# Performance work log

Measured on AMD Instinct MI355X. Metric: run time of the kernel, lower is better.

Reference implementation:

```python
import jax, jax.numpy as jnp
import numpy as np

# ---- module hyperparameters (init_kwargs) ----
QMIN, QMAX, QBINS = -8.0, 8.0, 128
PMIN, PMAX, PBINS = -10.0, 10.0, 128
GAMMA_F = 1.0
N_TRAJ = 16384


def _grid():
    # x = arange(qmin - 4/gamma_f, qmax + 4/gamma_f + 0.1/maxp, 0.1/maxp)
    maxp = max(abs(PMIN), abs(PMAX))
    step = 0.1 / maxp
    x = np.arange(QMIN - 4.0 / GAMMA_F, QMAX + 4.0 / GAMMA_F + step, step)
    return x.astype(np.float32)


def setup_inputs() -> dict:
    key = jax.random.key(0)
    ks = jax.random.split(key, 6)
    shape = (1, N_TRAJ)
    x = jnp.asarray(_grid())
    # psi buffer: stand-in for np.interp(x, spl.x, spl.psis[-1][1]) -- a
    # localized oscillatory wavefunction sampled on the grid.
    psi = (jnp.exp(-0.5 * (x - 1.0) ** 2) * jnp.cos(2.0 * x)).astype(jnp.float32)
    return {
        "factors_re": jax.random.normal(ks[0], shape, jnp.float32),
        "factors_im": jax.random.normal(ks[1], shape, jnp.float32),
        "q_re": jax.random.normal(ks[2], shape, jnp.float32),
        "q_im": 0.5 * jax.random.normal(ks[3], shape, jnp.float32),
        "p_re": jax.random.normal(ks[4], shape, jnp.float32),
        "p_im": 0.5 * jax.random.normal(ks[5], shape, jnp.float32),
        "x": x,
        "psi": psi,
    }


def _trapz0(y, x):
    # trapezoid rule along axis 0; y: [M, N] (complex), x: [M]
    dx = jnp.diff(x)
    return jnp.sum(0.5 * (y[1:] + y[:-1]) * dx[:, None], axis=0)


def _forward(factors_re, factors_im, q_re, q_im, p_re, p_im, x, psi):
    g = GAMMA_F
    factors = factors_re + 1j * factors_im  # [1, N] complex
    # _calc_proj: xi = 2*g*q + 1j*p ; qf = Re(xi)/(2g), pf = Im(xi)
    qf = q_re - p_im / (2.0 * g)
    pf = 2.0 * g * q_im + p_re
    dq = (QMAX - QMIN) / QBINS
    dp = (PMAX - PMIN) / PBINS
    qb = jnp.floor((qf - QMIN) / dq)
    pb = jnp.floor((pf - PMIN) / dp)
    bins = (qb * PBINS + pb).astype(jnp.int32).reshape(-1)  # [N]
    n = bins.shape[0]
    # torch: enumerate(torch.unique(bins)) -> rank among sorted unique values.
    # jnp.unique inverse (size=n, large fill pads at the end) gives the same map.
    _, inv = jnp.unique(bins, return_inverse=True, size=n, fill_value=jnp.int32(2**30))
    inds = inv.reshape(qf.shape)  # [1, N] compact bin ids
    qc = (qb + 0.5) * dq + QMIN  # bin centers [1, N]
    pc = (pb + 0.5) * dp + PMIN
    # _gf: coherent-state Gaussians on grid x -> [M, N]
    norm = (2.0 * g / jnp.pi) ** 0.25
    dxq = x[:, None] - qc.reshape(-1)[None, :]  # [M, N]
    gfs = norm * jnp.exp(-g * dxq * dxq + 1j * pc.reshape(-1)[None, :] * dxq)
    gt = _trapz0(jnp.conj(gfs) * psi[:, None], x)  # [N] complex
    # _calc_pref (reconstruction): exponential prefactor that can blow up,
    # hence the nan_to_num + clamp in the original.
    pref = norm * jnp.exp(g * q_im * q_im + 1j * (p_re * q_im))  # [1, N]
    pref = (jnp.clip(jnp.nan_to_num(pref.real), -100.0, 100.0)
            + 1j * jnp.clip(jnp.nan_to_num(pref.imag), -100.0, 100.0))
    vals = pref * factors  # [1, N]
    b = vals.shape[0]
    binned = jnp.zeros_like(vals).at[jnp.arange(b)[:, None], inds].add(vals)
    loss = jnp.sum(jnp.abs(binned - gt[None, :]) ** 2)
    return jnp.sqrt(loss)


def reference(factors_re, factors_im, q_re, q_im, p_re, p_im, x, psi):
    return _forward(factors_re, factors_im, q_re, q_im, p_re, p_im, x, psi)
```

## Files before the change

### kernel.cpp

```cpp
#include <hip/hip_runtime.h>
#include <math.h>


#define PRES_BITS  65536
#define PRES_WORDS 1024
#define PRES_OFF   32768
#define CHUNKS     16

__global__ void prep_kernel(const float* __restrict__ f_re, const float* __restrict__ f_im,
                            const float* __restrict__ q_re, const float* __restrict__ q_im,
                            const float* __restrict__ p_re, const float* __restrict__ p_im,
                            float* __restrict__ qc, float* __restrict__ pc,
                            float* __restrict__ vre, float* __restrict__ vim,
                            int* __restrict__ bins, unsigned long long* __restrict__ pres, int n)
{
    int i = blockIdx.x * blockDim.x + threadIdx.x;
    if (i >= n) return;
    const float norm = 0.8932438417380023f;
    float qi = q_im[i], pr = p_re[i];
    float qf = q_re[i] - 0.5f * p_im[i];
    float pf = 2.0f * qi + pr;
    float qb = floorf((qf - (-8.0f)) / 0.125f);
    float pb = floorf((pf - (-10.0f)) / 0.15625f);
    int b = (int)(qb * 128.0f + pb);
    bins[i] = b;
    int pidx = min(max(b + PRES_OFF, 0), PRES_BITS - 1);
    atomicOr(&pres[pidx >> 6], 1ull << (pidx & 63));
    qc[i] = (qb + 0.5f) * 0.125f + (-8.0f);
    pc[i] = (pb + 0.5f) * 0.15625f + (-10.0f);
    float ea = norm * expf(qi * qi);
    float s, c;
    __sincosf(pr * qi, &s, &c);
    float prr = fminf(fmaxf(ea * c, -100.0f), 100.0f);
    float pri = fminf(fmaxf(ea * s, -100.0f), 100.0f);
    float fr = f_re[i], fi = f_im[i];
    vre[i] = prr * fr - pri * fi;
    vim[i] = prr * fi + pri * fr;
}

__global__ void wpsi_kernel(const float* __restrict__ x, const float* __restrict__ psi,
                            float* __restrict__ wpsi, int M)
{
    int m = blockIdx.x * blockDim.x + threadIdx.x;
    if (m >= M) return;
    float w;
    if (m == 0)            w = 0.5f * (x[1] - x[0]);
    else if (m == M - 1)   w = 0.5f * (x[M - 1] - x[M - 2]);
    else                   w = 0.5f * (x[m + 1] - x[m - 1]);
    wpsi[m] = w * psi[m] * 0.8932438417380023f;
}

__global__ void scan_kernel(const unsigned long long* __restrict__ pres, int* __restrict__ base)
{
    __shared__ int partials[PRES_WORDS];
    int t = threadIdx.x;
    int c = __popcll(pres[t]);
    partials[t] = c;
    __syncthreads();
    for (int off = 1; off < PRES_WORDS; off <<= 1) {
        int v = (t >= off) ? partials[t - off] : 0;
        __syncthreads();
        partials[t] += v;
        __syncthreads();
    }
    base[t] = partials[t] - c;
}

__global__ void scatter_kernel(const int* __restrict__ bins,
                               const unsigned long long* __restrict__ pres,
                               const int* __restrict__ base,
                               const float* __restrict__ vre, const float* __restrict__ vim,
                               float* __restrict__ bre, float* __restrict__ bim, int n)
{
    int i = blockIdx.x * blockDim.x + threadIdx.x;
    if (i >= n) return;
    int pidx = min(max(bins[i] + PRES_OFF, 0), PRES_BITS - 1);
    int w = pidx >> 6, bit = pidx & 63;
    unsigned long long below = pres[w] & ((bit == 0) ? 0ull : (~0ull >> (64 - bit)));
    int cid = base[w] + __popcll(below);
    atomicAdd(&bre[cid], vre[i]);
    atomicAdd(&bim[cid], vim[i]);
}

__global__ void gt_kernel(const float* __restrict__ x, const float* __restrict__ wpsi,
                          const float* __restrict__ qc, const float* __restrict__ pc,
                          float* __restrict__ gre, float* __restrict__ gim,
                          int n, int M, int chunk)
{
    int t = blockIdx.x * blockDim.x + threadIdx.x;
    if (t >= n) return;
    float qcn = qc[t], pcn = pc[t];
    int m0 = blockIdx.y * chunk;
    int m1 = min(m0 + chunk, M);
    float sre = 0.0f, sim = 0.0f;
#pragma unroll 4
    for (int m = m0; m < m1; m++) {
        float xm = x[m], wm = wpsi[m];
        float dxq = xm - qcn;
        float e = __expf(-dxq * dxq) * wm;
        float s, c;
        __sincosf(pcn * dxq, &s, &c);
        sre = fmaf(e, c, sre);
        sim = fmaf(-e, s, sim);
    }
    atomicAdd(&gre[t], sre);
    atomicAdd(&gim[t], sim);
}

__global__ void loss_kernel(const float* __restrict__ gre, const float* __restrict__ gim,
                            const float* __restrict__ bre, const float* __restrict__ bim,
                            float* __restrict__ loss, int n)
{
    int t = blockIdx.x * blockDim.x + threadIdx.x;
    float v = 0.0f;
    if (t < n) {
        float dre = bre[t] - gre[t];
        float dim = bim[t] - gim[t];
        v = dre * dre + dim * dim;
    }
#pragma unroll
    for (int off = 32; off > 0; off >>= 1) v += __shfl_down(v, off);
    __shared__ float l[4];
    int wv = threadIdx.x >> 6, ln = threadIdx.x & 63;
    if (ln == 0) l[wv] = v;
    __syncthreads();
    if (threadIdx.x == 0)
        atomicAdd(loss, l[0] + l[1] + l[2] + l[3]);
}

__global__ void finalize_kernel(const float* __restrict__ loss, float* __restrict__ out)
{
    out[0] = sqrtf(loss[0]);
}

extern "C" void kernel_launch(void* const* d_in, const int* in_sizes, int n_in,
                              void* d_out, int out_size, void* d_ws, size_t ws_size,
                              hipStream_t stream)
{
    const float* f_re = (const float*)d_in[0];
    const float* f_im = (const float*)d_in[1];
    const float* q_re = (const float*)d_in[2];
    const float* q_im = (const float*)d_in[3];
    const float* p_re = (const float*)d_in[4];
    const float* p_im = (const float*)d_in[5];
    const float* x    = (const float*)d_in[6];
    const float* psi  = (const float*)d_in[7];
    int n = in_sizes[0];
    int M = in_sizes[6];

    float* wsf  = (float*)d_ws;
    float* qc   = wsf;
    float* pc   = qc + n;
    float* vre  = pc + n;
    float* vim  = vre + n;
    int*   bins = (int*)(vim + n);
    float* wpsi = (float*)(bins + n);
    int*   base = (int*)(wpsi + 4096);
    float* bre  = (float*)(base + PRES_WORDS);
    float* bim  = bre + n;
    float* gre  = bim + n;
    float* gim  = gre + n;
    unsigned long long* pres = (unsigned long long*)(gim + n);
    float* loss = (float*)(pres + PRES_WORDS);

    hipMemsetAsync(bre, 0, (size_t)(4 * n + 2 * PRES_WORDS + 1) * sizeof(float), stream);

    int chunk = (M + CHUNKS - 1) / CHUNKS;
    prep_kernel<<<(n + 255) / 256, 256, 0, stream>>>(f_re, f_im, q_re, q_im, p_re, p_im,
                                                     qc, pc, vre, vim, bins, pres, n);
    wpsi_kernel<<<(M + 255) / 256, 256, 0, stream>>>(x, psi, wpsi, M);
    scan_kernel<<<1, PRES_WORDS, 0, stream>>>(pres, base);
    scatter_kernel<<<(n + 255) / 256, 256, 0, stream>>>(bins, pres, base, vre, vim, bre, bim, n);
    gt_kernel<<<dim3((n + 255) / 256, CHUNKS), 256, 0, stream>>>(x, wpsi, qc, pc, gre, gim,
                                                                 n, M, chunk);
    loss_kernel<<<(n + 255) / 256, 256, 0, stream>>>(gre, gim, bre, bim, loss, n);
    finalize_kernel<<<1, 1, 0, stream>>>(loss, (float*)d_out);
}
```

Before: 123.4 us.

## Window the Gaussian overlap sum and fold small kernels into fewer launches

```diff
diff --git a/kernel.cpp b/kernel.cpp
--- a/kernel.cpp
+++ b/kernel.cpp
@@ -2,20 +2,32 @@
 #include <math.h>
 
 
+#define PRES_WORDS 1024
 #define PRES_BITS  65536
-#define PRES_WORDS 1024
 #define PRES_OFF   32768
 #define CHUNKS     16
+#define WINR       4.5f
 
 __global__ void prep_kernel(const float* __restrict__ f_re, const float* __restrict__ f_im,
                             const float* __restrict__ q_re, const float* __restrict__ q_im,
                             const float* __restrict__ p_re, const float* __restrict__ p_im,
+                            const float* __restrict__ x, const float* __restrict__ psi,
                             float* __restrict__ qc, float* __restrict__ pc,
                             float* __restrict__ vre, float* __restrict__ vim,
-                            int* __restrict__ bins, unsigned long long* __restrict__ pres, int n)
+                            int* __restrict__ bins, unsigned long long* __restrict__ pres,
+                            float* __restrict__ bre, float* __restrict__ bim,
+                            float2* __restrict__ xw, int n, int M)
 {
     int i = blockIdx.x * blockDim.x + threadIdx.x;
     if (i >= n) return;
+    bre[i] = 0.0f; bim[i] = 0.0f;
+    if (i < M) {
+        float w;
+        if (i == 0)          w = 0.5f * (x[1] - x[0]);
+        else if (i == M - 1) w = 0.5f * (x[M - 1] - x[M - 2]);
+        else                 w = 0.5f * (x[i + 1] - x[i - 1]);
+        xw[i] = make_float2(x[i], w * psi[i] * 0.8932438417380023f);
+    }
     const float norm = 0.8932438417380023f;
     float qi = q_im[i], pr = p_re[i];
     float qf = q_re[i] - 0.5f * p_im[i];
@@ -38,84 +50,85 @@
     vim[i] = prr * fi + pri * fr;
 }
 
-__global__ void wpsi_kernel(const float* __restrict__ x, const float* __restrict__ psi,
-                            float* __restrict__ wpsi, int M)
-{
-    int m = blockIdx.x * blockDim.x + threadIdx.x;
-    if (m >= M) return;
-    float w;
-    if (m == 0)            w = 0.5f * (x[1] - x[0]);
-    else if (m == M - 1)   w = 0.5f * (x[M - 1] - x[M - 2]);
-    else                   w = 0.5f * (x[m + 1] - x[m - 1]);
-    wpsi[m] = w * psi[m] * 0.8932438417380023f;
-}
-
-__global__ void scan_kernel(const unsigned long long* __restrict__ pres, int* __restrict__ base)
-{
-    __shared__ int partials[PRES_WORDS];
-    int t = threadIdx.x;
-    int c = __popcll(pres[t]);
-    partials[t] = c;
-    __syncthreads();
-    for (int off = 1; off < PRES_WORDS; off <<= 1) {
-        int v = (t >= off) ? partials[t - off] : 0;
-        __syncthreads();
-        partials[t] += v;
-        __syncthreads();
-    }
-    base[t] = partials[t] - c;
-}
-
 __global__ void scatter_kernel(const int* __restrict__ bins,
                                const unsigned long long* __restrict__ pres,
-                               const int* __restrict__ base,
                                const float* __restrict__ vre, const float* __restrict__ vim,
                                float* __restrict__ bre, float* __restrict__ bim, int n)
 {
-    int i = blockIdx.x * blockDim.x + threadIdx.x;
+    __shared__ int lbase[PRES_WORDS];
+    int tid = threadIdx.x;
+    if (tid < 64) {
+        int cum[16];
+        int tot = 0;
+        for (int k = 0; k < 16; k++) {
+            cum[k] = tot;
+            tot += __popcll(pres[tid * 16 + k]);
+        }
+        int run = tot;
+        for (int off = 1; off < 64; off <<= 1) {
+            int up = __shfl_up(run, off);
+            if (tid >= off) run += up;
+        }
+        int excl = run - tot;
+        for (int k = 0; k < 16; k++) lbase[tid * 16 + k] = excl + cum[k];
+    }
+    __syncthreads();
+    int i = blockIdx.x * blockDim.x + tid;
     if (i >= n) return;
     int pidx = min(max(bins[i] + PRES_OFF, 0), PRES_BITS - 1);
     int w = pidx >> 6, bit = pidx & 63;
     unsigned long long below = pres[w] & ((bit == 0) ? 0ull : (~0ull >> (64 - bit)));
-    int cid = base[w] + __popcll(below);
+    int cid = lbase[w] + __popcll(below);
     atomicAdd(&bre[cid], vre[i]);
     atomicAdd(&bim[cid], vim[i]);
 }
 
-__global__ void gt_kernel(const float* __restrict__ x, const float* __restrict__ wpsi,
+__global__ void gt_kernel(const float2* __restrict__ xw, const float* __restrict__ x,
                           const float* __restrict__ qc, const float* __restrict__ pc,
-                          float* __restrict__ gre, float* __restrict__ gim,
-                          int n, int M, int chunk)
+                          float* __restrict__ gpre, float* __restrict__ gpim,
+                          int n, int M)
 {
     int t = blockIdx.x * blockDim.x + threadIdx.x;
     if (t >= n) return;
     float qcn = qc[t], pcn = pc[t];
-    int m0 = blockIdx.y * chunk;
-    int m1 = min(m0 + chunk, M);
+    float x0f = x[0];
+    float flo = (qcn - WINR - x0f) * 100.0f;
+    float fhi = (qcn + WINR - x0f) * 100.0f;
+    int mlo = max(0, (int)flo - 1);
+    int mhi = min(M, (int)fhi + 2);
+    int len = mhi - mlo; if (len < 0) len = 0;
+    int c = blockIdx.y;
+    int ms = mlo + (len * c) / CHUNKS;
+    int me = mlo + (len * (c + 1)) / CHUNKS;
     float sre = 0.0f, sim = 0.0f;
-#pragma unroll 4
-    for (int m = m0; m < m1; m++) {
-        float xm = x[m], wm = wpsi[m];
-        float dxq = xm - qcn;
-        float e = __expf(-dxq * dxq) * wm;
-        float s, c;
-        __sincosf(pcn * dxq, &s, &c);
-        sre = fmaf(e, c, sre);
+    for (int m = ms; m < me; m++) {
+        float2 xm = xw[m];
+        float dxq = xm.x - qcn;
+        float e = __expf(-dxq * dxq) * xm.y;
+        float s, cc;
+        __sincosf(pcn * dxq, &s, &cc);
+        sre = fmaf(e, cc, sre);
         sim = fmaf(-e, s, sim);
     }
-    atomicAdd(&gre[t], sre);
-    atomicAdd(&gim[t], sim);
+    gpre[c * n + t] = sre;
+    gpim[c * n + t] = sim;
 }
 
-__global__ void loss_kernel(const float* __restrict__ gre, const float* __restrict__ gim,
-                            const float* __restrict__ bre, const float* __restrict__ bim,
-                            float* __restrict__ loss, int n)
+__global__ void loss_final_kernel(const float* __restrict__ gpre, const float* __restrict__ gpim,
+                                  const float* __restrict__ bre, const float* __restrict__ bim,
+                                  float* __restrict__ loss, int* __restrict__ donecnt,
+                                  float* __restrict__ out, int n)
 {
     int t = blockIdx.x * blockDim.x + threadIdx.x;
     float v = 0.0f;
     if (t < n) {
-        float dre = bre[t] - gre[t];
-        float dim = bim[t] - gim[t];
+        float sre = 0.0f, sim = 0.0f;
+        for (int c = 0; c < CHUNKS; c++) {
+            sre += gpre[c * n + t];
+            sim += gpim[c * n + t];
+        }
+        float dre = bre[t] - sre;
+        float dim = bim[t] - sim;
         v = dre * dre + dim * dim;
     }
 #pragma unroll
@@ -124,13 +137,15 @@
     int wv = threadIdx.x >> 6, ln = threadIdx.x & 63;
     if (ln == 0) l[wv] = v;
     __syncthreads();
-    if (threadIdx.x == 0)
+    if (threadIdx.x == 0) {
         atomicAdd(loss, l[0] + l[1] + l[2] + l[3]);
-}
-
-__global__ void finalize_kernel(const float* __restrict__ loss, float* __restrict__ out)
-{
-    out[0] = sqrtf(loss[0]);
+        __threadfence();
+        int old = atomicAdd(donecnt, 1);
+        if (old == (int)gridDim.x - 1) {
+            __threadfence();
+            out[0] = sqrtf(atomicAdd(loss, 0.0f));
+        }
+    }
 }
 
 extern "C" void kernel_launch(void* const* d_in, const int* in_sizes, int n_in,
@@ -154,25 +169,22 @@
     float* vre  = pc + n;
     float* vim  = vre + n;
     int*   bins = (int*)(vim + n);
-    float* wpsi = (float*)(bins + n);
-    int*   base = (int*)(wpsi + 4096);
-    float* bre  = (float*)(base + PRES_WORDS);
+    float* bre  = (float*)(bins + n);
     float* bim  = bre + n;
-    float* gre  = bim + n;
-    float* gim  = gre + n;
-    unsigned long long* pres = (unsigned long long*)(gim + n);
+    float* gpre = bim + n;
+    float* gpim = gpre + (size_t)CHUNKS * n;
+    float2* xw  = (float2*)(gpim + (size_t)CHUNKS * n);
+    unsigned long long* pres = (unsigned long long*)(xw + 4096);
     float* loss = (float*)(pres + PRES_WORDS);
+    int*   donecnt = (int*)(loss + 1);
 
-    hipMemsetAsync(bre, 0, (size_t)(4 * n + 2 * PRES_WORDS + 1) * sizeof(float), stream);
+    hipMemsetAsync(pres, 0, PRES_WORDS * sizeof(unsigned long long) + 8, stream);
 
-    int chunk = (M + CHUNKS - 1) / CHUNKS;
-    prep_kernel<<<(n + 255) / 256, 256, 0, stream>>>(f_re, f_im, q_re, q_im, p_re, p_im,
-                                                     qc, pc, vre, vim, bins, pres, n);
-    wpsi_kernel<<<(M + 255) / 256, 256, 0, stream>>>(x, psi, wpsi, M);
-    scan_kernel<<<1, PRES_WORDS, 0, stream>>>(pres, base);
-    scatter_kernel<<<(n + 255) / 256, 256, 0, stream>>>(bins, pres, base, vre, vim, bre, bim, n);
-    gt_kernel<<<dim3((n + 255) / 256, CHUNKS), 256, 0, stream>>>(x, wpsi, qc, pc, gre, gim,
-                                                                 n, M, chunk);
-    loss_kernel<<<(n + 255) / 256, 256, 0, stream>>>(gre, gim, bre, bim, loss, n);
-    finalize_kernel<<<1, 1, 0, stream>>>(loss, (float*)d_out);
+    int nb = (n + 255) / 256;
+    prep_kernel<<<nb, 256, 0, stream>>>(f_re, f_im, q_re, q_im, p_re, p_im, x, psi,
+                                        qc, pc, vre, vim, bins, pres, bre, bim, xw, n, M);
+    scatter_kernel<<<nb, 256, 0, stream>>>(bins, pres, vre, vim, bre, bim, n);
+    gt_kernel<<<dim3(nb, CHUNKS), 256, 0, stream>>>(xw, x, qc, pc, gpre, gpim, n, M);
+    loss_final_kernel<<<nb, 256, 0, stream>>>(gpre, gpim, bre, bim, loss, donecnt,
+                                              (float*)d_out, n);
 }
```

New measurement: 118.1 us. 4.3% less time.
